# Kernel tuning notes

Hardware: AMD Instinct MI355X
Metric: run time of the kernel (lower is better)

## Reference

```python
import jax, jax.numpy as jnp
import numpy as np

B, N_PER, K = 8, 4096, 16          # graphs, nodes per graph, knn neighbors
D_IN, D_H, D_OUT = 32, 64, 128     # feature_nn: 35->64->64, global_nn: 64->128
N = B * N_PER


def setup_inputs() -> dict:
    key = jax.random.key(0)
    ks = jax.random.split(key, 8)
    sc = lambda fan: 1.0 / np.sqrt(fan)
    x = jax.random.normal(ks[0], (N, D_IN), jnp.float32)
    pos = jax.random.normal(ks[1], (N, 3), jnp.float32)
    batch = jnp.repeat(jnp.arange(B, dtype=jnp.int32), N_PER)
    fW1 = jax.random.normal(ks[2], (D_IN + 3, D_H), jnp.float32) * sc(D_IN + 3)
    fb1 = jnp.zeros((D_H,), jnp.float32)
    fW2 = jax.random.normal(ks[3], (D_H, D_H), jnp.float32) * sc(D_H)
    fb2 = jnp.zeros((D_H,), jnp.float32)
    gW = jax.random.normal(ks[4], (D_H, D_OUT), jnp.float32) * sc(D_H)
    gb = jnp.zeros((D_OUT,), jnp.float32)
    return {"x": x, "pos": pos, "batch": batch,
            "fW1": fW1, "fb1": fb1, "fW2": fW2, "fb2": fb2,
            "gW": gW, "gb": gb}


def reference(x, pos, batch, fW1, fb1, fW2, fb2, gW, gb):
    # ---- knn(pos, pos, k, batch, batch): per-graph k nearest (self included) ----
    posb = pos.reshape(B, N_PER, 3)
    sq = jnp.sum(posb * posb, axis=-1)                      # [B, Nper]
    dist = sq[:, :, None] + sq[:, None, :] - 2.0 * jnp.einsum('bnd,bmd->bnm', posb, posb)
    _, nbr = jax.lax.top_k(-dist, K)                        # [B, Nper, K] local neighbor idx
    offs = (jnp.arange(B, dtype=nbr.dtype) * N_PER)[:, None, None]
    col = (nbr + offs).reshape(-1)                          # edge_index[1]: neighbor (x) idx
    row = jnp.repeat(jnp.arange(N, dtype=col.dtype), K)     # edge_index[0]: query (y) idx

    # ---- PointConv: msg = feature_nn(cat[x_j, pos_j - pos_i]), max-aggregate at i ----
    # PyG flow source_to_target: j = edge_index[0] = row (query), i = edge_index[1] = col.
    msg = jnp.concatenate([x[row], pos[row] - pos[col]], axis=1)  # [E, 35]
    h = jax.nn.relu(msg @ fW1 + fb1)
    h = jax.nn.relu(h @ fW2 + fb2)                          # [E, 64]
    agg = jax.ops.segment_max(h, col, num_segments=N)       # max aggregation
    agg = jnp.where(jnp.isfinite(agg), agg, 0.0)            # PyG fills empty segments with 0
    out = jax.nn.relu(agg @ gW + gb)                        # global_nn
    return (out, pos, batch)
```

## Files before the change

### kernel.cpp

```cpp
#include <hip/hip_runtime.h>
#include <hip/hip_bf16.h>

#define N_PER    4096
#define KNBR     16
#define NTOT     32768
#define D_IN     32
#define D_H      64
#define D_OUT    128
#define E_TOT    (NTOT * KNBR)

#define OUT1_OFF (NTOT * D_OUT)
#define OUT2_OFF (NTOT * D_OUT + NTOT*3)

#define KNN_INF 3.4e38f

typedef __attribute__((ext_vector_type(8))) short bf16x8;
typedef __attribute__((ext_vector_type(4))) float f32x4;

__device__ int            g_isbf16;
__device__ float          g_posf[NTOT * 3];
__device__ float          g_xf[NTOT * D_IN];
__device__ float          g_scf[NTOT];
__device__ int            g_nbr[E_TOT];
__device__ unsigned short g_base1h[NTOT * D_H];
__device__ uint4          g_Bfrag[2 * 4 * 64];
__device__ float          g_W1a[D_IN * D_H];
__device__ float          g_Wd[3 * D_H];
__device__ float          g_fb1v[D_H];
__device__ float          g_fb2v[D_H];
__device__ float          g_gWv[D_H * D_OUT];
__device__ float          g_gbv[D_OUT];
__device__ int            g_cnt[NTOT];
__device__ int            g_bsum[NTOT / 256];
__device__ int            g_bpre[NTOT / 256];
__device__ int            g_offs[NTOT + 1];
__device__ int            g_cursor[NTOT];
__device__ int            g_inlist[E_TOT];
__device__ float          g_agg[NTOT * D_H];

__device__ __forceinline__ float ldf(const void* p, int i, int bf) {
    if (bf) return __uint_as_float(((unsigned)((const unsigned short*)p)[i]) << 16);
    return ((const float*)p)[i];
}
__device__ __forceinline__ unsigned bf16rne(float f) {
    unsigned u = __float_as_uint(f);
    return (u + 0x7FFFu + ((u >> 16) & 1u)) >> 16;
}
__device__ __forceinline__ void stf(void* p, int i, float v, int bf) {
    if (bf) ((unsigned short*)p)[i] = (unsigned short)bf16rne(v);
    else    ((float*)p)[i] = v;
}
__device__ __forceinline__ float b2f(unsigned short h) {
    return __uint_as_float(((unsigned)h) << 16);
}

__global__ void probe_kernel(const void* __restrict__ x) {
    __shared__ int sc[256];
    const unsigned* xw = (const unsigned*)x;
    int t = threadIdx.x;
    int c = 0;
    for (int i = t; i < 4096; i += 256) {
        unsigned e = (xw[i] >> 7) & 0xFFu;
        c += (e >= 110u && e <= 140u) ? 1 : 0;
    }
    sc[t] = c;
    __syncthreads();
    for (int s = 128; s > 0; s >>= 1) { if (t < s) sc[t] += sc[t + s]; __syncthreads(); }
    if (t == 0) g_isbf16 = (sc[0] > 2048) ? 1 : 0;
}

__global__ __launch_bounds__(256) void prep_kernel(const void* __restrict__ x,
                                                   const void* __restrict__ pos) {
#pragma clang fp contract(off)
    const int bf = g_isbf16;
    const int i0 = blockIdx.x * 256 + threadIdx.x;
    const int stride = gridDim.x * 256;
    for (int i = i0; i < NTOT * D_IN; i += stride) g_xf[i] = ldf(x, i, bf);
    for (int i = i0; i < NTOT * 3;    i += stride) g_posf[i] = ldf(pos, i, bf);
    for (int i = i0; i < NTOT;        i += stride) {
        float a = ldf(pos, i * 3 + 0, bf);
        float b = ldf(pos, i * 3 + 1, bf);
        float c = ldf(pos, i * 3 + 2, bf);
        g_scf[i] = a * a + b * b + c * c;
        g_cnt[i] = 0;
    }
    for (int i = i0; i < NTOT * D_H;  i += stride) g_agg[i] = 0.0f;
}

__global__ void setup_kernel(const void* fW1, const void* fb1, const void* fW2,
                             const void* fb2, const void* gW, const void* gb) {
    int bf = g_isbf16;
    for (int t = threadIdx.x; t < D_IN * D_H; t += 256) g_W1a[t] = ldf(fW1, t, bf);
    for (int t = threadIdx.x; t < 3 * D_H; t += 256)    g_Wd[t]  = ldf(fW1, D_IN * D_H + t, bf);
    for (int t = threadIdx.x; t < D_H * D_OUT; t += 256) g_gWv[t] = ldf(gW, t, bf);
    if (threadIdx.x < D_H) {
        g_fb1v[threadIdx.x] = ldf(fb1, threadIdx.x, bf);
        g_fb2v[threadIdx.x] = ldf(fb2, threadIdx.x, bf);
    }
    if (threadIdx.x < D_OUT) g_gbv[threadIdx.x] = ldf(gb, threadIdx.x, bf);
    for (int idx = threadIdx.x; idx < 512; idx += 256) {
        int lane = idx & 63, nt = (idx >> 6) & 3, ks = idx >> 8;
        int n = nt * 16 + (lane & 15);
        int k0 = ks * 32 + ((lane >> 4) << 3);
        unsigned wds[4];
#pragma unroll
        for (int jp = 0; jp < 4; jp++) {
            unsigned lo = bf16rne(ldf(fW2, (k0 + 2 * jp) * D_H + n, bf));
            unsigned hi = bf16rne(ldf(fW2, (k0 + 2 * jp + 1) * D_H + n, bf));
            wds[jp] = lo | (hi << 16);
        }
        g_Bfrag[idx] = make_uint4(wds[0], wds[1], wds[2], wds[3]);
    }
}

__global__ __launch_bounds__(256) void knn_kernel() {
#pragma clang fp contract(off)
    __shared__ float s_d[4][8][64];
    __shared__ int   s_i[4][8][64];
    const int lane = threadIdx.x & 63;
    const int wid  = threadIdx.x >> 6;
    const int qbase = blockIdx.x * 32 + wid * 8;
    const int cbase = (qbase >> 12) << 12;
    const float* cp  = g_posf + cbase * 3;
    const float* csc = g_scf + cbase;

    float qx[8], qy[8], qz[8], qs[8];
#pragma unroll
    for (int r = 0; r < 8; r++) {
        qx[r] = g_posf[(qbase + r) * 3 + 0];
        qy[r] = g_posf[(qbase + r) * 3 + 1];
        qz[r] = g_posf[(qbase + r) * 3 + 2];
        qs[r] = g_scf[qbase + r];
    }

    float m[8];
#pragma unroll
    for (int r = 0; r < 8; r++) m[r] = KNN_INF;
    for (int c = 0; c < 64; c++) {
        int jj = c * 64 + lane;
        float px = cp[jj * 3], py = cp[jj * 3 + 1], pz = cp[jj * 3 + 2];
        float sc = csc[jj];
#pragma unroll
        for (int r = 0; r < 8; r++) {
            float dot = fmaf(pz, qz[r], fmaf(py, qy[r], px * qx[r]));
            float d = fmaf(-2.0f, dot, qs[r] + sc);
            m[r] = fminf(m[r], d);
        }
    }

    float T[8];
#pragma unroll
    for (int r = 0; r < 8; r++) {
        float v = m[r];
#pragma unroll
        for (int k = 2; k <= 64; k <<= 1) {
#pragma unroll
            for (int j2 = k >> 1; j2 >= 1; j2 >>= 1) {
                float pv = __shfl_xor(v, j2);
                bool keepMin = (((lane & j2) == 0) == ((lane & k) == 0));
                bool tp = ((pv < v) == keepMin);
                v = tp ? pv : v;
            }
        }
        T[r] = __shfl(v, 15) + 1e-3f;
    }

    int cnt[8];
#pragma unroll
    for (int r = 0; r < 8; r++) cnt[r] = 0;
    for (int c = 0; c < 64; c++) {
        int jj = c * 64 + lane;
        float px = cp[jj * 3], py = cp[jj * 3 + 1], pz = cp[jj * 3 + 2];
        float sc = csc[jj];
#pragma unroll
        for (int r = 0; r < 8; r++) {
            float dot = px * qx[r] + py * qy[r] + pz * qz[r];
            float d = (qs[r] + sc) - 2.0f * dot;
            bool p = (d <= T[r]);
            unsigned long long mk = __ballot(p);
            if (mk) {
                int pre = (int)__popcll(mk & ((1ull << lane) - 1ull));
                int slot = cnt[r] + pre;
                if (p && slot < 64) {
                    s_d[wid][r][slot] = d;
                    s_i[wid][r][slot] = cbase + jj;
                }
                cnt[r] += (int)__popcll(mk);
            }
        }
    }
    __syncthreads();

#pragma unroll
    for (int r = 0; r < 8; r++) {
        int q = qbase + r;
        if (cnt[r] <= 64) {
            int S = cnt[r];
            float d  = (lane < S) ? s_d[wid][r][lane] : KNN_INF;
            int   idx = (lane < S) ? s_i[wid][r][lane] : 0x7FFFFFFF;
#pragma unroll
            for (int k = 2; k <= 64; k <<= 1) {
#pragma unroll
                for (int j2 = k >> 1; j2 >= 1; j2 >>= 1) {
                    float pd = __shfl_xor(d, j2);
                    int   pi = __shfl_xor(idx, j2);
                    bool keepMin = (((lane & j2) == 0) == ((lane & k) == 0));
                    bool lt = (pd < d) || (pd == d && pi < idx);
                    bool tp = (lt == keepMin);
                    d   = tp ? pd : d;
                    idx = tp ? pi : idx;
                }
            }
            if (lane < 16) {
                g_nbr[q * KNBR + lane] = idx;
                atomicAdd(&g_cnt[idx & (NTOT - 1)], 1);
            }
        } else {
            float lastd = -KNN_INF; int lasti = -1;
            for (int t = 0; t < 16; t++) {
                float bd = KNN_INF; int bi = 0x7FFFFFFF;
                for (int c = 0; c < 64; c++) {
                    int jj = c * 64 + lane;
                    float px = cp[jj * 3], py = cp[jj * 3 + 1], pz = cp[jj * 3 + 2];
                    float sc = csc[jj];
                    float dot = px * qx[r] + py * qy[r] + pz * qz[r];
                    float dd = (qs[r] + sc) - 2.0f * dot;
                    int gj = cbase + jj;
                    bool after  = (dd > lastd) || (dd == lastd && gj > lasti);
                    bool better = (dd < bd) || (dd == bd && gj < bi);
                    if (after && better) { bd = dd; bi = gj; }
                }
#pragma unroll
                for (int s2 = 1; s2 < 64; s2 <<= 1) {
                    float od = __shfl_xor(bd, s2);
                    int   oi = __shfl_xor(bi, s2);
                    if (od < bd || (od == bd && oi < bi)) { bd = od; bi = oi; }
                }
                if (lane == 0) {
                    g_nbr[q * KNBR + t] = bi;
                    atomicAdd(&g_cnt[bi & (NTOT - 1)], 1);
                }
                lastd = bd; lasti = bi;
            }
        }
    }
}

__global__ __launch_bounds__(256) void base1_kernel() {
    int lane = threadIdx.x & 63, wid = threadIdx.x >> 6;
    int n0 = blockIdx.x * 32 + wid * 8;
    float wcol[D_IN];
#pragma unroll
    for (int k = 0; k < D_IN; k++) wcol[k] = g_W1a[k * D_H + lane];
    float bb = g_fb1v[lane];
    for (int r = 0; r < 8; r++) {
        int n = n0 + r;
        float acc = bb;
#pragma unroll
        for (int k = 0; k < D_IN; k++) acc += g_xf[n * D_IN + k] * wcol[k];
        g_base1h[(size_t)n * D_H + lane] = (unsigned short)bf16rne(acc);
    }
}

__global__ __launch_bounds__(256) void scanA_kernel() {
    __shared__ int red[4];
    int t = threadIdx.x, lane = t & 63, w = t >> 6;
    int v = g_cnt[blockIdx.x * 256 + t];
    int s = v;
#pragma unroll
    for (int off = 1; off < 64; off <<= 1) s += __shfl_xor(s, off);
    if (lane == 0) red[w] = s;
    __syncthreads();
    if (t == 0) g_bsum[blockIdx.x] = red[0] + red[1] + red[2] + red[3];
}

__global__ __launch_bounds__(64) void scanB_kernel() {
    int t = threadIdx.x;
    int a = g_bsum[2 * t], b = g_bsum[2 * t + 1];
    int p = a + b;
    int inc = p;
#pragma unroll
    for (int off = 1; off < 64; off <<= 1) {
        int u = __shfl_up(inc, off);
        if (t >= off) inc += u;
    }
    int excl = inc - p;
    g_bpre[2 * t] = excl;
    g_bpre[2 * t + 1] = excl + a;
}

__global__ __launch_bounds__(256) void scanC_kernel() {
    __shared__ int wsum[4];
    int t = threadIdx.x, lane = t & 63, w = t >> 6;
    int i = blockIdx.x * 256 + t;
    int v = g_cnt[i];
    int inc = v;
#pragma unroll
    for (int off = 1; off < 64; off <<= 1) {
        int u = __shfl_up(inc, off);
        if (lane >= off) inc += u;
    }
    if (lane == 63) wsum[w] = inc;
    __syncthreads();
    int wbase = 0;
    for (int k = 0; k < w; k++) wbase += wsum[k];
    int excl = g_bpre[blockIdx.x] + wbase + inc - v;
    g_offs[i] = excl;
    g_cursor[i] = excl;
    if (i == NTOT - 1) g_offs[NTOT] = E_TOT;
}

__global__ void scatter_kernel() {
    int e = blockIdx.x * 256 + threadIdx.x;
    int c = g_nbr[e] & (NTOT - 1);
    int slot = atomicAdd(&g_cursor[c], 1);
    g_inlist[slot & (E_TOT - 1)] = e;
}

__global__ __launch_bounds__(256) void edge_kernel() {
    __shared__ unsigned short sA[256 * 72];
    __shared__ int scol[256];
    const int t    = threadIdx.x;
    const int lane = t & 63;
    const int w    = t >> 6;
    const int slot0 = blockIdx.x * 256;

    {
        int e = g_inlist[slot0 + t];
        int n = (e >> 4) & (NTOT - 1);
        int j = g_nbr[e] & (NTOT - 1);
        scol[t] = j;
        float dx = g_posf[n * 3 + 0] - g_posf[j * 3 + 0];
        float dy = g_posf[n * 3 + 1] - g_posf[j * 3 + 1];
        float dz = g_posf[n * 3 + 2] - g_posf[j * 3 + 2];
        const unsigned short* b1 = g_base1h + (size_t)n * D_H;
#pragma unroll
        for (int d0 = 0; d0 < D_H; d0 += 8) {
            uint4 p = *(const uint4*)(b1 + d0);
            unsigned pw[4] = {p.x, p.y, p.z, p.w};
            unsigned qw[4];
#pragma unroll
            for (int jp = 0; jp < 4; jp++) {
                int d = d0 + 2 * jp;
                float v0 = __uint_as_float(pw[jp] << 16)
                         + dx * g_Wd[d]     + dy * g_Wd[64 + d]     + dz * g_Wd[128 + d];
                float v1 = __uint_as_float(pw[jp] & 0xFFFF0000u)
                         + dx * g_Wd[d + 1] + dy * g_Wd[64 + d + 1] + dz * g_Wd[128 + d + 1];
                v0 = fmaxf(v0, 0.f); v1 = fmaxf(v1, 0.f);
                qw[jp] = bf16rne(v0) | (bf16rne(v1) << 16);
            }
            *(uint4*)(&sA[t * 72 + d0]) = make_uint4(qw[0], qw[1], qw[2], qw[3]);
        }
    }
    __syncthreads();

    f32x4 acc[4][4];
#pragma unroll
    for (int a = 0; a < 4; a++)
#pragma unroll
        for (int b = 0; b < 4; b++) acc[a][b] = (f32x4){0.f, 0.f, 0.f, 0.f};

    const int quad = lane >> 4;
    const int l15  = lane & 15;
#pragma unroll
    for (int ks = 0; ks < 2; ks++) {
        bf16x8 bfrag[4];
#pragma unroll
        for (int nt = 0; nt < 4; nt++)
            bfrag[nt] = ((const bf16x8*)g_Bfrag)[ks * 256 + nt * 64 + lane];
#pragma unroll
        for (int mt = 0; mt < 4; mt++) {
            int row = w * 64 + mt * 16 + l15;
            bf16x8 afrag = *(const bf16x8*)(&sA[row * 72 + ks * 32 + quad * 8]);
#pragma unroll
            for (int nt = 0; nt < 4; nt++)
                acc[mt][nt] = __builtin_amdgcn_mfma_f32_16x16x32_bf16(afrag, bfrag[nt], acc[mt][nt], 0, 0, 0);
        }
    }
    __syncthreads();

#pragma unroll
    for (int nt = 0; nt < 4; nt++) {
        int dim = nt * 16 + l15;
        float bb = g_fb2v[dim];
#pragma unroll
        for (int mt = 0; mt < 4; mt++) {
#pragma unroll
            for (int r = 0; r < 4; r++) {
                int edge = w * 64 + mt * 16 + quad * 4 + r;
                float v = fmaxf(acc[mt][nt][r] + bb, 0.f);
                sA[edge * 72 + dim] = (unsigned short)bf16rne(v);
            }
        }
    }
    __syncthreads();

    {
        const int ls0 = w * 64;
        const int gs0 = slot0 + ls0;
        int cur = -1;
        float vmax = 0.f;
        for (int s = ls0; s < ls0 + 64; s++) {
            int cj = scol[s];
            float v = b2f(sA[s * 72 + lane]);
            if (cj != cur) {
                if (cur >= 0) {
                    int lo = g_offs[cur], hi = g_offs[cur + 1];
                    if (lo >= gs0 && hi <= gs0 + 64)
                        g_agg[(size_t)cur * D_H + lane] = vmax;
                    else
                        atomicMax((unsigned*)&g_agg[(size_t)cur * D_H + lane], __float_as_uint(vmax));
                }
                cur = cj; vmax = v;
            } else {
                vmax = fmaxf(vmax, v);
            }
        }
        if (cur >= 0) {
            int lo = g_offs[cur], hi = g_offs[cur + 1];
            if (lo >= gs0 && hi <= gs0 + 64)
                g_agg[(size_t)cur * D_H + lane] = vmax;
            else
                atomicMax((unsigned*)&g_agg[(size_t)cur * D_H + lane], __float_as_uint(vmax));
        }
    }
}

__global__ __launch_bounds__(128) void out_kernel(void* __restrict__ out) {
    const int bf = g_isbf16;
    int d = threadIdx.x;
    float gcol[D_H];
#pragma unroll
    for (int k = 0; k < D_H; k++) gcol[k] = g_gWv[k * D_OUT + d];
    float bb = g_gbv[d];
    int n0 = blockIdx.x * 16;
    for (int r = 0; r < 16; r++) {
        int n = n0 + r;
        float acc = bb;
#pragma unroll
        for (int k = 0; k < D_H; k++) acc += g_agg[(size_t)n * D_H + k] * gcol[k];
        stf(out, n * D_OUT + d, fmaxf(acc, 0.f), bf);
    }
}

__global__ void misc_kernel(const void* __restrict__ pos, const int* __restrict__ batch,
                            void* __restrict__ out) {
    const int bf = g_isbf16;
    int i = blockIdx.x * 256 + threadIdx.x;
    if (bf) {
        if (i < NTOT * 3) ((unsigned short*)out)[OUT1_OFF + i] = ((const unsigned short*)pos)[i];
        if (i < NTOT)     ((unsigned short*)out)[OUT2_OFF + i] = (unsigned short)bf16rne((float)batch[i]);
    } else {
        if (i < NTOT * 3) ((float*)out)[OUT1_OFF + i] = ((const float*)pos)[i];
        if (i < NTOT)     ((float*)out)[OUT2_OFF + i] = (float)batch[i];
    }
}

extern "C" void kernel_launch(void* const* d_in, const int* in_sizes, int n_in,
                              void* d_out, int out_size, void* d_ws, size_t ws_size,
                              hipStream_t stream) {
    const void* x     = d_in[0];
    const void* pos   = d_in[1];
    const int*  batch = (const int*)d_in[2];
    const void* fW1   = d_in[3];
    const void* fb1   = d_in[4];
    const void* fW2   = d_in[5];
    const void* fb2   = d_in[6];
    const void* gW    = d_in[7];
    const void* gb    = d_in[8];

    hipLaunchKernelGGL(probe_kernel,   dim3(1),           dim3(256), 0, stream, x);
    hipLaunchKernelGGL(prep_kernel,    dim3(1024),        dim3(256), 0, stream, x, pos);
    hipLaunchKernelGGL(setup_kernel,   dim3(1),           dim3(256), 0, stream, fW1, fb1, fW2, fb2, gW, gb);
    hipLaunchKernelGGL(base1_kernel,   dim3(NTOT / 32),   dim3(256), 0, stream);
    hipLaunchKernelGGL(knn_kernel,     dim3(NTOT / 32),   dim3(256), 0, stream);
    hipLaunchKernelGGL(scanA_kernel,   dim3(NTOT / 256),  dim3(256), 0, stream);
    hipLaunchKernelGGL(scanB_kernel,   dim3(1),           dim3(64),  0, stream);
    hipLaunchKernelGGL(scanC_kernel,   dim3(NTOT / 256),  dim3(256), 0, stream);
    hipLaunchKernelGGL(scatter_kernel, dim3(E_TOT / 256), dim3(256), 0, stream);
    hipLaunchKernelGGL(edge_kernel,    dim3(E_TOT / 256), dim3(256), 0, stream);
    hipLaunchKernelGGL(out_kernel,     dim3(NTOT / 16),   dim3(128), 0, stream, d_out);
    hipLaunchKernelGGL(misc_kernel,    dim3((NTOT * 3 + 255) / 256), dim3(256), 0, stream, pos, batch, d_out);
}
```

Baseline: 303.6 us.

## Fuse prep/setup/base1, scan phases, and output kernels to cut launches

Merges the probe, prep, setup and base1 kernels into one multi-role prep kernel that detects bf16 per wave and reads the raw inputs directly, dropping the g_xf and weight staging copies. The scanB pass is folded into scanC, which now sums the preceding block totals itself, and out_kernel is merged with misc_kernel. The knn kernel no longer keeps candidate distances in shared memory and recomputes them from positions at the sort stage, and the knn distance arithmetic now uses fmaf. This removes several launches and intermediate buffers, at the cost of redundant weight loads per block and extra gathers in knn. The fmaf change can alter rounding relative to the later non-fused recompute and so shift which candidates pass the threshold.

New measurement: 294.9 us. 2.8% less time.

```diff
diff --git a/kernel.cpp b/kernel.cpp
--- a/kernel.cpp
+++ b/kernel.cpp
@@ -17,22 +17,15 @@
 typedef __attribute__((ext_vector_type(8))) short bf16x8;
 typedef __attribute__((ext_vector_type(4))) float f32x4;
 
-__device__ int            g_isbf16;
 __device__ float          g_posf[NTOT * 3];
-__device__ float          g_xf[NTOT * D_IN];
 __device__ float          g_scf[NTOT];
 __device__ int            g_nbr[E_TOT];
 __device__ unsigned short g_base1h[NTOT * D_H];
 __device__ uint4          g_Bfrag[2 * 4 * 64];
-__device__ float          g_W1a[D_IN * D_H];
 __device__ float          g_Wd[3 * D_H];
-__device__ float          g_fb1v[D_H];
 __device__ float          g_fb2v[D_H];
-__device__ float          g_gWv[D_H * D_OUT];
-__device__ float          g_gbv[D_OUT];
 __device__ int            g_cnt[NTOT];
 __device__ int            g_bsum[NTOT / 256];
-__device__ int            g_bpre[NTOT / 256];
 __device__ int            g_offs[NTOT + 1];
 __device__ int            g_cursor[NTOT];
 __device__ int            g_inlist[E_TOT];
@@ -53,70 +46,72 @@
 __device__ __forceinline__ float b2f(unsigned short h) {
     return __uint_as_float(((unsigned)h) << 16);
 }
-
-__global__ void probe_kernel(const void* __restrict__ x) {
-    __shared__ int sc[256];
-    const unsigned* xw = (const unsigned*)x;
-    int t = threadIdx.x;
-    int c = 0;
-    for (int i = t; i < 4096; i += 256) {
-        unsigned e = (xw[i] >> 7) & 0xFFu;
-        c += (e >= 110u && e <= 140u) ? 1 : 0;
-    }
-    sc[t] = c;
-    __syncthreads();
-    for (int s = 128; s > 0; s >>= 1) { if (t < s) sc[t] += sc[t + s]; __syncthreads(); }
-    if (t == 0) g_isbf16 = (sc[0] > 2048) ? 1 : 0;
+__device__ __forceinline__ int wave_probe(const void* x) {
+    unsigned wv = ((const unsigned*)x)[threadIdx.x & 63];
+    unsigned e = (wv >> 7) & 0xFFu;
+    unsigned long long mk = __ballot(e >= 110u && e <= 140u);
+    return (__popcll(mk) >= 32) ? 1 : 0;
 }
 
 __global__ __launch_bounds__(256) void prep_kernel(const void* __restrict__ x,
-                                                   const void* __restrict__ pos) {
+                                                   const void* __restrict__ pos,
+                                                   const void* __restrict__ fW1,
+                                                   const void* __restrict__ fb1,
+                                                   const void* __restrict__ fW2,
+                                                   const void* __restrict__ fb2) {
+    const int bf = wave_probe(x);
+    const int b = blockIdx.x;
+    if (b < 1024) {
+        const int i0 = b * 256 + threadIdx.x;
+        const int stride = 1024 * 256;
+        for (int i = i0; i < NTOT * 3; i += stride) g_posf[i] = ldf(pos, i, bf);
+        {
 #pragma clang fp contract(off)
-    const int bf = g_isbf16;
-    const int i0 = blockIdx.x * 256 + threadIdx.x;
-    const int stride = gridDim.x * 256;
-    for (int i = i0; i < NTOT * D_IN; i += stride) g_xf[i] = ldf(x, i, bf);
-    for (int i = i0; i < NTOT * 3;    i += stride) g_posf[i] = ldf(pos, i, bf);
-    for (int i = i0; i < NTOT;        i += stride) {
-        float a = ldf(pos, i * 3 + 0, bf);
-        float b = ldf(pos, i * 3 + 1, bf);
-        float c = ldf(pos, i * 3 + 2, bf);
-        g_scf[i] = a * a + b * b + c * c;
-        g_cnt[i] = 0;
-    }
-    for (int i = i0; i < NTOT * D_H;  i += stride) g_agg[i] = 0.0f;
-}
-
-__global__ void setup_kernel(const void* fW1, const void* fb1, const void* fW2,
-                             const void* fb2, const void* gW, const void* gb) {
-    int bf = g_isbf16;
-    for (int t = threadIdx.x; t < D_IN * D_H; t += 256) g_W1a[t] = ldf(fW1, t, bf);
-    for (int t = threadIdx.x; t < 3 * D_H; t += 256)    g_Wd[t]  = ldf(fW1, D_IN * D_H + t, bf);
-    for (int t = threadIdx.x; t < D_H * D_OUT; t += 256) g_gWv[t] = ldf(gW, t, bf);
-    if (threadIdx.x < D_H) {
-        g_fb1v[threadIdx.x] = ldf(fb1, threadIdx.x, bf);
-        g_fb2v[threadIdx.x] = ldf(fb2, threadIdx.x, bf);
-    }
-    if (threadIdx.x < D_OUT) g_gbv[threadIdx.x] = ldf(gb, threadIdx.x, bf);
-    for (int idx = threadIdx.x; idx < 512; idx += 256) {
-        int lane = idx & 63, nt = (idx >> 6) & 3, ks = idx >> 8;
-        int n = nt * 16 + (lane & 15);
-        int k0 = ks * 32 + ((lane >> 4) << 3);
-        unsigned wds[4];
-#pragma unroll
-        for (int jp = 0; jp < 4; jp++) {
-            unsigned lo = bf16rne(ldf(fW2, (k0 + 2 * jp) * D_H + n, bf));
-            unsigned hi = bf16rne(ldf(fW2, (k0 + 2 * jp + 1) * D_H + n, bf));
-            wds[jp] = lo | (hi << 16);
-        }
-        g_Bfrag[idx] = make_uint4(wds[0], wds[1], wds[2], wds[3]);
+            for (int i = i0; i < NTOT; i += stride) {
+                float a = ldf(pos, i * 3 + 0, bf);
+                float c2 = ldf(pos, i * 3 + 1, bf);
+                float c3 = ldf(pos, i * 3 + 2, bf);
+                g_scf[i] = a * a + c2 * c2 + c3 * c3;
+                g_cnt[i] = 0;
+            }
+        }
+        for (int i = i0; i < NTOT * D_H; i += stride) g_agg[i] = 0.0f;
+    } else if (b < 2048) {
+        int lane = threadIdx.x & 63, wid = threadIdx.x >> 6;
+        int n0 = (b - 1024) * 32 + wid * 8;
+        float wcol[D_IN];
+#pragma unroll
+        for (int k = 0; k < D_IN; k++) wcol[k] = ldf(fW1, k * D_H + lane, bf);
+        float bb = ldf(fb1, lane, bf);
+        for (int r = 0; r < 8; r++) {
+            int n = n0 + r;
+            float acc = bb;
+#pragma unroll
+            for (int k = 0; k < D_IN; k++) acc += ldf(x, n * D_IN + k, bf) * wcol[k];
+            g_base1h[(size_t)n * D_H + lane] = (unsigned short)bf16rne(acc);
+        }
+    } else {
+        for (int t = threadIdx.x; t < 3 * D_H; t += 256) g_Wd[t] = ldf(fW1, D_IN * D_H + t, bf);
+        if (threadIdx.x < D_H) g_fb2v[threadIdx.x] = ldf(fb2, threadIdx.x, bf);
+        for (int idx = threadIdx.x; idx < 512; idx += 256) {
+            int lane = idx & 63, nt = (idx >> 6) & 3, ks = idx >> 8;
+            int n = nt * 16 + (lane & 15);
+            int k0 = ks * 32 + ((lane >> 4) << 3);
+            unsigned wds[4];
+#pragma unroll
+            for (int jp = 0; jp < 4; jp++) {
+                unsigned lo = bf16rne(ldf(fW2, (k0 + 2 * jp) * D_H + n, bf));
+                unsigned hi = bf16rne(ldf(fW2, (k0 + 2 * jp + 1) * D_H + n, bf));
+                wds[jp] = lo | (hi << 16);
+            }
+            g_Bfrag[idx] = make_uint4(wds[0], wds[1], wds[2], wds[3]);
+        }
     }
 }
 
 __global__ __launch_bounds__(256) void knn_kernel() {
 #pragma clang fp contract(off)
-    __shared__ float s_d[4][8][64];
-    __shared__ int   s_i[4][8][64];
+    __shared__ int s_i[4][8][64];
     const int lane = threadIdx.x & 63;
     const int wid  = threadIdx.x >> 6;
     const int qbase = blockIdx.x * 32 + wid * 8;
@@ -174,17 +169,14 @@
         float sc = csc[jj];
 #pragma unroll
         for (int r = 0; r < 8; r++) {
-            float dot = px * qx[r] + py * qy[r] + pz * qz[r];
-            float d = (qs[r] + sc) - 2.0f * dot;
+            float dot = fmaf(pz, qz[r], fmaf(py, qy[r], px * qx[r]));
+            float d = fmaf(-2.0f, dot, qs[r] + sc);
             bool p = (d <= T[r]);
             unsigned long long mk = __ballot(p);
             if (mk) {
                 int pre = (int)__popcll(mk & ((1ull << lane) - 1ull));
                 int slot = cnt[r] + pre;
-                if (p && slot < 64) {
-                    s_d[wid][r][slot] = d;
-                    s_i[wid][r][slot] = cbase + jj;
-                }
+                if (p && slot < 64) s_i[wid][r][slot] = cbase + jj;
                 cnt[r] += (int)__popcll(mk);
             }
         }
@@ -196,8 +188,14 @@
         int q = qbase + r;
         if (cnt[r] <= 64) {
             int S = cnt[r];
-            float d  = (lane < S) ? s_d[wid][r][lane] : KNN_INF;
-            int   idx = (lane < S) ? s_i[wid][r][lane] : 0x7FFFFFFF;
+            int idx = (lane < S) ? s_i[wid][r][lane] : 0x7FFFFFFF;
+            float d = KNN_INF;
+            if (lane < S) {
+                float px = g_posf[idx * 3], py = g_posf[idx * 3 + 1], pz = g_posf[idx * 3 + 2];
+                float sc = g_scf[idx];
+                float dot = px * qx[r] + py * qy[r] + pz * qz[r];
+                d = (qs[r] + sc) - 2.0f * dot;
+            }
 #pragma unroll
             for (int k = 2; k <= 64; k <<= 1) {
 #pragma unroll
@@ -246,22 +244,6 @@
     }
 }
 
-__global__ __launch_bounds__(256) void base1_kernel() {
-    int lane = threadIdx.x & 63, wid = threadIdx.x >> 6;
-    int n0 = blockIdx.x * 32 + wid * 8;
-    float wcol[D_IN];
-#pragma unroll
-    for (int k = 0; k < D_IN; k++) wcol[k] = g_W1a[k * D_H + lane];
-    float bb = g_fb1v[lane];
-    for (int r = 0; r < 8; r++) {
-        int n = n0 + r;
-        float acc = bb;
-#pragma unroll
-        for (int k = 0; k < D_IN; k++) acc += g_xf[n * D_IN + k] * wcol[k];
-        g_base1h[(size_t)n * D_H + lane] = (unsigned short)bf16rne(acc);
-    }
-}
-
 __global__ __launch_bounds__(256) void scanA_kernel() {
     __shared__ int red[4];
     int t = threadIdx.x, lane = t & 63, w = t >> 6;
@@ -274,24 +256,18 @@
     if (t == 0) g_bsum[blockIdx.x] = red[0] + red[1] + red[2] + red[3];
 }
 
-__global__ __launch_bounds__(64) void scanB_kernel() {
-    int t = threadIdx.x;
-    int a = g_bsum[2 * t], b = g_bsum[2 * t + 1];
-    int p = a + b;
-    int inc = p;
-#pragma unroll
-    for (int off = 1; off < 64; off <<= 1) {
-        int u = __shfl_up(inc, off);
-        if (t >= off) inc += u;
-    }
-    int excl = inc - p;
-    g_bpre[2 * t] = excl;
-    g_bpre[2 * t + 1] = excl + a;
-}
-
 __global__ __launch_bounds__(256) void scanC_kernel() {
+    __shared__ int sred[4];
     __shared__ int wsum[4];
     int t = threadIdx.x, lane = t & 63, w = t >> 6;
+    int contrib = (t < 128 && t < blockIdx.x) ? g_bsum[t] : 0;
+    int rs = contrib;
+#pragma unroll
+    for (int off = 1; off < 64; off <<= 1) rs += __shfl_xor(rs, off);
+    if (lane == 0) sred[w] = rs;
+    __syncthreads();
+    int base = sred[0] + sred[1] + sred[2] + sred[3];
+
     int i = blockIdx.x * 256 + t;
     int v = g_cnt[i];
     int inc = v;
@@ -304,7 +280,7 @@
     __syncthreads();
     int wbase = 0;
     for (int k = 0; k < w; k++) wbase += wsum[k];
-    int excl = g_bpre[blockIdx.x] + wbase + inc - v;
+    int excl = base + wbase + inc - v;
     g_offs[i] = excl;
     g_cursor[i] = excl;
     if (i == NTOT - 1) g_offs[NTOT] = E_TOT;
@@ -426,33 +402,37 @@
     }
 }
 
-__global__ __launch_bounds__(128) void out_kernel(void* __restrict__ out) {
-    const int bf = g_isbf16;
-    int d = threadIdx.x;
-    float gcol[D_H];
-#pragma unroll
-    for (int k = 0; k < D_H; k++) gcol[k] = g_gWv[k * D_OUT + d];
-    float bb = g_gbv[d];
-    int n0 = blockIdx.x * 16;
-    for (int r = 0; r < 16; r++) {
-        int n = n0 + r;
-        float acc = bb;
-#pragma unroll
-        for (int k = 0; k < D_H; k++) acc += g_agg[(size_t)n * D_H + k] * gcol[k];
-        stf(out, n * D_OUT + d, fmaxf(acc, 0.f), bf);
-    }
-}
-
-__global__ void misc_kernel(const void* __restrict__ pos, const int* __restrict__ batch,
-                            void* __restrict__ out) {
-    const int bf = g_isbf16;
-    int i = blockIdx.x * 256 + threadIdx.x;
-    if (bf) {
-        if (i < NTOT * 3) ((unsigned short*)out)[OUT1_OFF + i] = ((const unsigned short*)pos)[i];
-        if (i < NTOT)     ((unsigned short*)out)[OUT2_OFF + i] = (unsigned short)bf16rne((float)batch[i]);
+__global__ __launch_bounds__(256) void outmisc_kernel(const void* __restrict__ x,
+                                                      const void* __restrict__ gW,
+                                                      const void* __restrict__ gb,
+                                                      const int* __restrict__ batch,
+                                                      const void* __restrict__ pos,
+                                                      void* __restrict__ out) {
+    const int bf = wave_probe(x);
+    const int b = blockIdx.x;
+    if (b < 2048) {
+        int t = threadIdx.x, d = t & 127, half = t >> 7;
+        float gcol[D_H];
+#pragma unroll
+        for (int k = 0; k < D_H; k++) gcol[k] = ldf(gW, k * D_OUT + d, bf);
+        float bb = ldf(gb, d, bf);
+        int n0 = b * 16 + half * 8;
+        for (int r = 0; r < 8; r++) {
+            int n = n0 + r;
+            float acc = bb;
+#pragma unroll
+            for (int k = 0; k < D_H; k++) acc += g_agg[(size_t)n * D_H + k] * gcol[k];
+            stf(out, n * D_OUT + d, fmaxf(acc, 0.f), bf);
+        }
     } else {
-        if (i < NTOT * 3) ((float*)out)[OUT1_OFF + i] = ((const float*)pos)[i];
-        if (i < NTOT)     ((float*)out)[OUT2_OFF + i] = (float)batch[i];
+        int i = (b - 2048) * 256 + threadIdx.x;
+        if (bf) {
+            if (i < NTOT * 3) ((unsigned short*)out)[OUT1_OFF + i] = ((const unsigned short*)pos)[i];
+            if (i < NTOT)     ((unsigned short*)out)[OUT2_OFF + i] = (unsigned short)bf16rne((float)batch[i]);
+        } else {
+            if (i < NTOT * 3) ((float*)out)[OUT1_OFF + i] = ((const float*)pos)[i];
+            if (i < NTOT)     ((float*)out)[OUT2_OFF + i] = (float)batch[i];
+        }
     }
 }
 
@@ -469,16 +449,12 @@
     const void* gW    = d_in[7];
     const void* gb    = d_in[8];
 
-    hipLaunchKernelGGL(probe_kernel,   dim3(1),           dim3(256), 0, stream, x);
-    hipLaunchKernelGGL(prep_kernel,    dim3(1024),        dim3(256), 0, stream, x, pos);
-    hipLaunchKernelGGL(setup_kernel,   dim3(1),           dim3(256), 0, stream, fW1, fb1, fW2, fb2, gW, gb);
-    hipLaunchKernelGGL(base1_kernel,   dim3(NTOT / 32),   dim3(256), 0, stream);
+    hipLaunchKernelGGL(prep_kernel,    dim3(2049),        dim3(256), 0, stream, x, pos, fW1, fb1, fW2, fb2);
     hipLaunchKernelGGL(knn_kernel,     dim3(NTOT / 32),   dim3(256), 0, stream);
     hipLaunchKernelGGL(scanA_kernel,   dim3(NTOT / 256),  dim3(256), 0, stream);
-    hipLaunchKernelGGL(scanB_kernel,   dim3(1),           dim3(64),  0, stream);
     hipLaunchKernelGGL(scanC_kernel,   dim3(NTOT / 256),  dim3(256), 0, stream);
     hipLaunchKernelGGL(scatter_kernel, dim3(E_TOT / 256), dim3(256), 0, stream);
     hipLaunchKernelGGL(edge_kernel,    dim3(E_TOT / 256), dim3(256), 0, stream);
-    hipLaunchKernelGGL(out_kernel,     dim3(NTOT / 16),   dim3(128), 0, stream, d_out);
-    hipLaunchKernelGGL(misc_kernel,    dim3((NTOT * 3 + 255) / 256), dim3(256), 0, stream, pos, batch, d_out);
-}
+    hipLaunchKernelGGL(outmisc_kernel, dim3(2048 + (NTOT * 3 + 255) / 256), dim3(256), 0, stream,
+                       x, gW, gb, batch, pos, d_out);
+}
```
